# Kernel optimization log

Hardware: AMD Instinct MI355X
Metric: run time of the kernel (lower is better)

The kernel has to match this reference:

```python
import jax, jax.numpy as jnp
import numpy as np

MINI = 1e-6
B, V, K, D = 256, 4096, 64, 10000


def setup_inputs() -> dict:
    key = jax.random.key(0)
    ks = jax.random.split(key, 7)
    batch_BOW = jax.random.randint(ks[0], (B, V), 0, 4, dtype=jnp.int32)
    batch_indices = jax.random.randint(ks[1], (B,), 0, D, dtype=jnp.int64)
    # Gamma-distributed priors as in __init__
    alpha = jax.random.gamma(ks[2], 10.0, (K,)).astype(jnp.float32)
    pi = jax.random.gamma(ks[3], 10.0, (D, K)).astype(jnp.float32)
    beta = (jax.random.gamma(ks[4], 2.0, (V, K)) / 100.0).astype(jnp.float32)
    exp_m = jax.random.uniform(ks[5], (D, K), dtype=jnp.float32)
    exp_m = exp_m / exp_m.sum(axis=1, keepdims=True)  # row-normalized as in __init__
    exp_n = jax.random.uniform(ks[6], (V, K), dtype=jnp.float32)
    exp_n = exp_n / exp_n.sum(axis=1, keepdims=True)
    return {
        "batch_BOW": batch_BOW,
        "batch_indices": batch_indices,
        "alpha": alpha,
        "pi": pi,
        "exp_m": exp_m,
        "beta": beta,
        "exp_n": exp_n,
        "iter_n": 10,
        "C_m": 1000000,
        "batch_C": 25000,
    }


def reference(batch_BOW, batch_indices, alpha, pi, exp_m, beta, exp_n, iter_n, C_m, batch_C):
    # Vectorized SCVB0 E-step (gather nonzero BOW, gamma responsibilities, scatter-accumulate).
    cnt = batch_BOW.astype(alpha.dtype)                      # [B,V]
    mask = (batch_BOW > 0).astype(alpha.dtype)               # [B,V]
    theta = alpha[None, :] * pi[batch_indices] + exp_m[batch_indices]   # [B,K]
    beta_sum = beta.sum(axis=0)                              # [K]
    exp_n_sum = exp_n.sum(axis=0)                            # [K]
    phi = (beta + exp_n) / (beta_sum + exp_n_sum)            # [V,K]
    gamma = theta[:, None, :] * phi[None, :, :] * mask[:, :, None]      # [B,V,K]
    gamma = gamma / (gamma.sum(axis=-1, keepdims=True) + MINI)
    # scatter-accumulate counts
    temp_exp_n = jnp.einsum('bvk,bv->vk', gamma, cnt)        # [V,K]
    temp_exp_m = jnp.einsum('bvk,bv->bk', gamma, cnt)        # [B,K]
    # entropy term: zero rows contribute 0 (0 * log eps = 0), matching nonzero-only loop
    exp_q_z = jnp.sum(gamma * jnp.log(gamma + MINI))
    # stochastic VI update
    rho = 1.0 / (iter_n + 5) ** 0.9
    new_exp_m_batch = (1.0 - rho) * exp_m[batch_indices] + rho * temp_exp_m
    new_exp_n = (1.0 - rho) * exp_n + rho * temp_exp_n * (C_m / batch_C)
    return temp_exp_n, temp_exp_m, exp_q_z, new_exp_n, new_exp_m_batch
```

## Files before the change

### kernel.cpp

```cpp
#include <hip/hip_runtime.h>
#include <math.h>

#define B_ 256
#define V_ 4096
#define K_ 64
#define MINI 1e-6f

#define TEN_OFF 0
#define TEM_OFF (V_*K_)
#define QZ_OFF  (TEM_OFF + B_*K_)
#define NEN_OFF (QZ_OFF + 1)
#define NEM_OFF (NEN_OFF + V_*K_)

#define WS_RHO    64
#define WS_SCALE  65
#define WS_PART   128
#define WS_ENT    4352
#define WS_TENP   8192
#define WS_TEMP   (WS_TENP + 4*V_*K_)

__device__ __forceinline__ int detect_is64(const int* bi) {
    int any = 0;
#pragma unroll
    for (int i = 1; i < 64; i += 2) any |= bi[i];
    return any == 0;
}

__device__ __forceinline__ float wave_sum64(float x) {
    x += __shfl_xor(x, 1);
    x += __shfl_xor(x, 2);
    x += __shfl_xor(x, 4);
    x += __shfl_xor(x, 8);
    x += __shfl_xor(x, 16);
    x += __shfl_xor(x, 32);
    return x;
}

__global__ __launch_bounds__(256) void k_pre(
    const float* __restrict__ beta, const float* __restrict__ exp_n,
    const int* __restrict__ iterp, const int* __restrict__ cmp,
    const int* __restrict__ bcp, float* __restrict__ ws)
{
    const int blk = blockIdx.x, tid = threadIdx.x;
    if (blk < 64) {
        __shared__ float red[256];
        const int k = tid & 63, sub = tid >> 6;
        float p = 0.f;
#pragma unroll
        for (int i = 0; i < 16; i++) {
            const int v = blk * 64 + sub * 16 + i;
            p += beta[v * K_ + k] + exp_n[v * K_ + k];
        }
        red[tid] = p;
        __syncthreads();
        if (tid < 64)
            ws[WS_PART + blk * 64 + tid] =
                red[tid] + red[64 + tid] + red[128 + tid] + red[192 + tid];
    } else {
        if (tid == 0) {
            ws[WS_RHO] = powf((float)(iterp[0] + 5), -0.9f);
            ws[WS_SCALE] = (float)cmp[0] / (float)bcp[0];
        }
    }
}

__global__ __launch_bounds__(256, 1) void k_main(
    const int* __restrict__ BOW, const int* __restrict__ bidx,
    const float* __restrict__ alpha, const float* __restrict__ pi,
    const float* __restrict__ exp_m, const float* __restrict__ beta,
    const float* __restrict__ exp_n,
    float* __restrict__ ws)
{
    __shared__ float th_s[64 * 68];
    __shared__ float ph_s[64 * 68];
    __shared__ float phl_s[64 * 68];
    __shared__ float wtl_s[64 * 68];
    __shared__ unsigned char cnt_s[64 * 65];
    __shared__ float dred[256];
    __shared__ float rden_s[64];
    __shared__ float entw[4];
    __shared__ int is64s;
    const int tid = threadIdx.x;
    const int vt = blockIdx.x & 63, bt = blockIdx.x >> 6;
    const int b0 = bt * 64, v0 = vt * 64;

    if (tid == 0) is64s = detect_is64(bidx);
    {
        const int k = tid & 63, g0 = tid >> 6;
        float s = 0.f;
#pragma unroll
        for (int i = 0; i < 16; i++)
            s += ws[WS_PART + (g0 + 4 * i) * 64 + k];
        dred[tid] = s;
    }
    __syncthreads();
    if (tid < 64)
        rden_s[tid] = __builtin_amdgcn_rcpf(
            dred[tid] + dred[64 + tid] + dred[128 + tid] + dred[192 + tid]);
    __syncthreads();

    {
        const int r = tid >> 2, q = tid & 3;
        const int idx = is64s ? bidx[2 * (b0 + r)] : bidx[b0 + r];
        const int v = v0 + r;
#pragma unroll
        for (int c4 = 0; c4 < 4; c4++) {
            const int k = q * 16 + c4 * 4;
            const float4 a4 = *(const float4*)&alpha[k];
            const float4 p4 = *(const float4*)&pi[idx * K_ + k];
            const float4 m4 = *(const float4*)&exp_m[idx * K_ + k];
            float4 t, tl;
            t.x = a4.x * p4.x + m4.x;  tl.x = t.x * __logf(t.x);
            t.y = a4.y * p4.y + m4.y;  tl.y = t.y * __logf(t.y);
            t.z = a4.z * p4.z + m4.z;  tl.z = t.z * __logf(t.z);
            t.w = a4.w * p4.w + m4.w;  tl.w = t.w * __logf(t.w);
            *(float4*)&th_s[r * 68 + k]  = t;
            *(float4*)&wtl_s[r * 68 + k] = tl;
            const float4 b4 = *(const float4*)&beta[v * K_ + k];
            const float4 e4 = *(const float4*)&exp_n[v * K_ + k];
            const float4 d4 = *(const float4*)&rden_s[k];
            float4 p, pl;
            p.x = (b4.x + e4.x) * d4.x;  pl.x = p.x * __logf(p.x);
            p.y = (b4.y + e4.y) * d4.y;  pl.y = p.y * __logf(p.y);
            p.z = (b4.z + e4.z) * d4.z;  pl.z = p.z * __logf(p.z);
            p.w = (b4.w + e4.w) * d4.w;  pl.w = p.w * __logf(p.w);
            *(float4*)&ph_s[r * 68 + k]  = p;
            *(float4*)&phl_s[r * 68 + k] = pl;
            const int4 cc = *(const int4*)&BOW[(b0 + r) * V_ + v0 + k];
            cnt_s[r * 65 + k + 0] = (unsigned char)cc.x;
            cnt_s[r * 65 + k + 1] = (unsigned char)cc.y;
            cnt_s[r * 65 + k + 2] = (unsigned char)cc.z;
            cnt_s[r * 65 + k + 3] = (unsigned char)cc.w;
        }
    }
    __syncthreads();

    const int tb = tid & 15, tv = tid >> 4;
    float s_acc[4][4] = {}, e_acc[4][4] = {};
    for (int kk = 0; kk < 64; kk += 4) {
        float4 at[4], al[4], bp[4], bl[4];
#pragma unroll
        for (int i = 0; i < 4; i++) {
            at[i] = *(const float4*)&th_s [(tb + 16 * i) * 68 + kk];
            al[i] = *(const float4*)&wtl_s[(tb + 16 * i) * 68 + kk];
        }
#pragma unroll
        for (int j = 0; j < 4; j++) {
            bp[j] = *(const float4*)&ph_s [(tv + 16 * j) * 68 + kk];
            bl[j] = *(const float4*)&phl_s[(tv + 16 * j) * 68 + kk];
        }
#pragma unroll
        for (int i = 0; i < 4; i++)
#pragma unroll
            for (int j = 0; j < 4; j++) {
                s_acc[i][j] += at[i].x * bp[j].x + at[i].y * bp[j].y
                             + at[i].z * bp[j].z + at[i].w * bp[j].w;
                e_acc[i][j] += al[i].x * bp[j].x + al[i].y * bp[j].y
                             + al[i].z * bp[j].z + al[i].w * bp[j].w
                             + at[i].x * bl[j].x + at[i].y * bl[j].y
                             + at[i].z * bl[j].z + at[i].w * bl[j].w;
            }
    }
    __syncthreads();

    float ent = 0.f;
#pragma unroll
    for (int i = 0; i < 4; i++)
#pragma unroll
        for (int j = 0; j < 4; j++) {
            const int bi = tb + 16 * i, vj = tv + 16 * j;
            const float s = s_acc[i][j];
            const float sm = s + MINI;
            const float r = __builtin_amdgcn_rcpf(sm);
            const int c = (int)cnt_s[bi * 65 + vj];
            wtl_s[bi * 68 + vj] = (float)c * r;
            if (c) ent += (e_acc[i][j] - s * __logf(sm)) * r;
        }
    ent = wave_sum64(ent);
    if ((tid & 63) == 0) entw[tid >> 6] = ent;
    __syncthreads();
    if (tid == 0)
        ws[WS_ENT + blockIdx.x] = entw[0] + entw[1] + entw[2] + entw[3];

    {
        const int tk = tid & 15, tv2 = tid >> 4;
        float ta[4][4] = {};
        for (int b = 0; b < 64; b++) {
            const float4 wv = *(const float4*)&wtl_s[b * 68 + 4 * tv2];
            const float4 t4 = *(const float4*)&th_s[b * 68 + 4 * tk];
            const float* wp = &wv.x;
            const float* tp = &t4.x;
#pragma unroll
            for (int j = 0; j < 4; j++)
#pragma unroll
                for (int c = 0; c < 4; c++) ta[j][c] += wp[j] * tp[c];
        }
#pragma unroll
        for (int j = 0; j < 4; j++) {
            const int v = 4 * tv2 + j;
            float4 o;
            o.x = ta[j][0] * ph_s[v * 68 + 4 * tk + 0];
            o.y = ta[j][1] * ph_s[v * 68 + 4 * tk + 1];
            o.z = ta[j][2] * ph_s[v * 68 + 4 * tk + 2];
            o.w = ta[j][3] * ph_s[v * 68 + 4 * tk + 3];
            *(float4*)&ws[WS_TENP + bt * (V_ * K_) + (v0 + v) * K_ + 4 * tk] = o;
        }
    }

    {
        const int tk = tid & 15, tb2 = tid >> 4;
        float Z[4][4] = {};
        for (int v = 0; v < 64; v++) {
            const float4 p4 = *(const float4*)&ph_s[v * 68 + 4 * tk];
            const float* pp = &p4.x;
#pragma unroll
            for (int i = 0; i < 4; i++) {
                const float w = wtl_s[(4 * tb2 + i) * 68 + v];
#pragma unroll
                for (int c = 0; c < 4; c++) Z[i][c] += w * pp[c];
            }
        }
#pragma unroll
        for (int i = 0; i < 4; i++) {
            const int b = 4 * tb2 + i;
            float4 o;
            o.x = th_s[b * 68 + 4 * tk + 0] * Z[i][0];
            o.y = th_s[b * 68 + 4 * tk + 1] * Z[i][1];
            o.z = th_s[b * 68 + 4 * tk + 2] * Z[i][2];
            o.w = th_s[b * 68 + 4 * tk + 3] * Z[i][3];
            *(float4*)&ws[WS_TEMP + blockIdx.x * 4096 + b * K_ + 4 * tk] = o;
        }
    }
}

__global__ __launch_bounds__(256) void k_post(
    const int* __restrict__ bidx, const float* __restrict__ exp_n,
    const float* __restrict__ exp_m, const float* __restrict__ ws,
    float* __restrict__ out)
{
    const int blk = blockIdx.x, tid = threadIdx.x;
    if (blk < 256) {
        const float rho = ws[WS_RHO];
        const int t = blk * 256 + tid;
        const float4 p0 = *(const float4*)&ws[WS_TENP + 0 * (V_ * K_) + t * 4];
        const float4 p1 = *(const float4*)&ws[WS_TENP + 1 * (V_ * K_) + t * 4];
        const float4 p2 = *(const float4*)&ws[WS_TENP + 2 * (V_ * K_) + t * 4];
        const float4 p3 = *(const float4*)&ws[WS_TENP + 3 * (V_ * K_) + t * 4];
        float4 s;
        s.x = (p0.x + p1.x) + (p2.x + p3.x);
        s.y = (p0.y + p1.y) + (p2.y + p3.y);
        s.z = (p0.z + p1.z) + (p2.z + p3.z);
        s.w = (p0.w + p1.w) + (p2.w + p3.w);
        *(float4*)&out[TEN_OFF + t * 4] = s;
        const float4 e4 = *(const float4*)&exp_n[t * 4];
        const float rs = rho * ws[WS_SCALE];
        out[NEN_OFF + t * 4 + 0] = (1.f - rho) * e4.x + rs * s.x;
        out[NEN_OFF + t * 4 + 1] = (1.f - rho) * e4.y + rs * s.y;
        out[NEN_OFF + t * 4 + 2] = (1.f - rho) * e4.z + rs * s.z;
        out[NEN_OFF + t * 4 + 3] = (1.f - rho) * e4.w + rs * s.w;
    } else if (blk < 320) {
        __shared__ int is64s;
        if (tid == 0) is64s = detect_is64(bidx);
        __syncthreads();
        const float rho = ws[WS_RHO];
        const int b = (blk - 256) * 4 + (tid >> 6);
        const int k = tid & 63;
        const int bt = b >> 6, r = b & 63;
        float s = 0.f;
#pragma unroll 8
        for (int vt = 0; vt < 64; vt++)
            s += ws[WS_TEMP + (vt * 4 + bt) * 4096 + r * K_ + k];
        out[TEM_OFF + b * K_ + k] = s;
        const int idx = is64s ? bidx[2 * b] : bidx[b];
        out[NEM_OFF + b * K_ + k] =
            (1.f - rho) * exp_m[idx * K_ + k] + rho * s;
    } else {
        __shared__ float red[256];
        red[tid] = ws[WS_ENT + tid];
        __syncthreads();
        for (int s = 128; s > 0; s >>= 1) {
            if (tid < s) red[tid] += red[tid + s];
            __syncthreads();
        }
        if (tid == 0) out[QZ_OFF] = red[0];
    }
}

extern "C" void kernel_launch(void* const* d_in, const int* in_sizes, int n_in,
                              void* d_out, int out_size, void* d_ws, size_t ws_size,
                              hipStream_t stream)
{
    const int*   BOW   = (const int*)d_in[0];
    const int*   bidx  = (const int*)d_in[1];
    const float* alpha = (const float*)d_in[2];
    const float* pi    = (const float*)d_in[3];
    const float* exp_m = (const float*)d_in[4];
    const float* beta  = (const float*)d_in[5];
    const float* exp_n = (const float*)d_in[6];
    const int*   iterp = (const int*)d_in[7];
    const int*   cmp   = (const int*)d_in[8];
    const int*   bcp   = (const int*)d_in[9];
    float* out = (float*)d_out;
    float* ws  = (float*)d_ws;

    hipLaunchKernelGGL(k_pre, dim3(65), dim3(256), 0, stream,
                       beta, exp_n, iterp, cmp, bcp, ws);
    hipLaunchKernelGGL(k_main, dim3(256), dim3(256), 0, stream,
                       BOW, bidx, alpha, pi, exp_m, beta, exp_n, ws);
    hipLaunchKernelGGL(k_post, dim3(321), dim3(256), 0, stream,
                       bidx, exp_n, exp_m, ws, out);
}
```

Before: 103.5 us.

## Move main-kernel GEMMs onto bf16 MFMA instructions with transposed LDS tiles

Replaces the three scalar FP32 register-tiled mini-GEMMs in k_main (the normalizer/entropy product, the vocab-side accumulation and the doc-side accumulation) with 16x16x32 bf16 MFMA intrinsics. Theta, phi and their x·log(x) terms are stored to LDS as truncated bf16, along with transposed copies so that each MFMA operand fragment is a contiguous 8-element load. The weight matrix W is written in both orientations. The aim is to move the block's FMA-bound inner loops onto the matrix cores. In exchange the products use bf16-truncated operands, which lowers accuracy and may break tolerance. Outputs are now written as scattered scalar stores, and LDS footprint grows.

```diff
diff --git a/kernel.cpp b/kernel.cpp
--- a/kernel.cpp
+++ b/kernel.cpp
@@ -18,6 +18,15 @@
 #define WS_ENT    4352
 #define WS_TENP   8192
 #define WS_TEMP   (WS_TENP + 4*V_*K_)
+
+#define LDB 72
+
+typedef __attribute__((ext_vector_type(8))) short bf16x8;
+typedef __attribute__((ext_vector_type(4))) float f32x4;
+
+__device__ __forceinline__ short bf(float x) {
+    return (short)(__float_as_uint(x) >> 16);
+}
 
 __device__ __forceinline__ int detect_is64(const int* bi) {
     int any = 0;
@@ -34,6 +43,10 @@
     x += __shfl_xor(x, 16);
     x += __shfl_xor(x, 32);
     return x;
+}
+
+__device__ __forceinline__ bf16x8 ldfrag(const short* arr, int row, int kofs) {
+    return *(const bf16x8*)&arr[row * LDB + kofs];
 }
 
 __global__ __launch_bounds__(256) void k_pre(
@@ -71,10 +84,16 @@
     const float* __restrict__ exp_n,
     float* __restrict__ ws)
 {
-    __shared__ float th_s[64 * 68];
-    __shared__ float ph_s[64 * 68];
-    __shared__ float phl_s[64 * 68];
-    __shared__ float wtl_s[64 * 68];
+    __shared__ __align__(16) float th_s[64 * 68];
+    __shared__ __align__(16) float ph_s[64 * 68];
+    __shared__ __align__(16) short th_b [64 * LDB];
+    __shared__ __align__(16) short thl_b[64 * LDB];
+    __shared__ __align__(16) short ph_b [64 * LDB];
+    __shared__ __align__(16) short phl_b[64 * LDB];
+    __shared__ __align__(16) short tht_b[64 * LDB];
+    __shared__ __align__(16) short pht_b[64 * LDB];
+    __shared__ __align__(16) short W_b  [64 * LDB];
+    __shared__ __align__(16) short Wt_b [64 * LDB];
     __shared__ unsigned char cnt_s[64 * 65];
     __shared__ float dred[256];
     __shared__ float rden_s[64];
@@ -114,8 +133,13 @@
             t.y = a4.y * p4.y + m4.y;  tl.y = t.y * __logf(t.y);
             t.z = a4.z * p4.z + m4.z;  tl.z = t.z * __logf(t.z);
             t.w = a4.w * p4.w + m4.w;  tl.w = t.w * __logf(t.w);
-            *(float4*)&th_s[r * 68 + k]  = t;
-            *(float4*)&wtl_s[r * 68 + k] = tl;
+            *(float4*)&th_s[r * 68 + k] = t;
+            *(short4*)&th_b [r * LDB + k] = make_short4(bf(t.x), bf(t.y), bf(t.z), bf(t.w));
+            *(short4*)&thl_b[r * LDB + k] = make_short4(bf(tl.x), bf(tl.y), bf(tl.z), bf(tl.w));
+            tht_b[(k + 0) * LDB + r] = bf(t.x);
+            tht_b[(k + 1) * LDB + r] = bf(t.y);
+            tht_b[(k + 2) * LDB + r] = bf(t.z);
+            tht_b[(k + 3) * LDB + r] = bf(t.w);
             const float4 b4 = *(const float4*)&beta[v * K_ + k];
             const float4 e4 = *(const float4*)&exp_n[v * K_ + k];
             const float4 d4 = *(const float4*)&rden_s[k];
@@ -124,8 +148,13 @@
             p.y = (b4.y + e4.y) * d4.y;  pl.y = p.y * __logf(p.y);
             p.z = (b4.z + e4.z) * d4.z;  pl.z = p.z * __logf(p.z);
             p.w = (b4.w + e4.w) * d4.w;  pl.w = p.w * __logf(p.w);
-            *(float4*)&ph_s[r * 68 + k]  = p;
-            *(float4*)&phl_s[r * 68 + k] = pl;
+            *(float4*)&ph_s[r * 68 + k] = p;
+            *(short4*)&ph_b [r * LDB + k] = make_short4(bf(p.x), bf(p.y), bf(p.z), bf(p.w));
+            *(short4*)&phl_b[r * LDB + k] = make_short4(bf(pl.x), bf(pl.y), bf(pl.z), bf(pl.w));
+            pht_b[(k + 0) * LDB + r] = bf(p.x);
+            pht_b[(k + 1) * LDB + r] = bf(p.y);
+            pht_b[(k + 2) * LDB + r] = bf(p.z);
+            pht_b[(k + 3) * LDB + r] = bf(p.w);
             const int4 cc = *(const int4*)&BOW[(b0 + r) * V_ + v0 + k];
             cnt_s[r * 65 + k + 0] = (unsigned char)cc.x;
             cnt_s[r * 65 + k + 1] = (unsigned char)cc.y;
@@ -135,100 +164,92 @@
     }
     __syncthreads();
 
-    const int tb = tid & 15, tv = tid >> 4;
-    float s_acc[4][4] = {}, e_acc[4][4] = {};
-    for (int kk = 0; kk < 64; kk += 4) {
-        float4 at[4], al[4], bp[4], bl[4];
-#pragma unroll
-        for (int i = 0; i < 4; i++) {
-            at[i] = *(const float4*)&th_s [(tb + 16 * i) * 68 + kk];
-            al[i] = *(const float4*)&wtl_s[(tb + 16 * i) * 68 + kk];
-        }
+    const int lane = tid & 63, wv = tid >> 6;
+    const int l15 = lane & 15, quad = lane >> 4;
+    const int qk = quad * 8;
+
+    {
+        const int mb = wv * 16;
+        const bf16x8 a_t0 = ldfrag(th_b,  mb + l15, 0  + qk);
+        const bf16x8 a_t1 = ldfrag(th_b,  mb + l15, 32 + qk);
+        const bf16x8 a_l0 = ldfrag(thl_b, mb + l15, 0  + qk);
+        const bf16x8 a_l1 = ldfrag(thl_b, mb + l15, 32 + qk);
+        float entacc = 0.f;
 #pragma unroll
         for (int j = 0; j < 4; j++) {
-            bp[j] = *(const float4*)&ph_s [(tv + 16 * j) * 68 + kk];
-            bl[j] = *(const float4*)&phl_s[(tv + 16 * j) * 68 + kk];
-        }
-#pragma unroll
-        for (int i = 0; i < 4; i++)
-#pragma unroll
-            for (int j = 0; j < 4; j++) {
-                s_acc[i][j] += at[i].x * bp[j].x + at[i].y * bp[j].y
-                             + at[i].z * bp[j].z + at[i].w * bp[j].w;
-                e_acc[i][j] += al[i].x * bp[j].x + al[i].y * bp[j].y
-                             + al[i].z * bp[j].z + al[i].w * bp[j].w
-                             + at[i].x * bl[j].x + at[i].y * bl[j].y
-                             + at[i].z * bl[j].z + at[i].w * bl[j].w;
+            const int vrow = j * 16 + l15;
+            const bf16x8 b_p0 = ldfrag(ph_b,  vrow, 0  + qk);
+            const bf16x8 b_p1 = ldfrag(ph_b,  vrow, 32 + qk);
+            const bf16x8 b_l0 = ldfrag(phl_b, vrow, 0  + qk);
+            const bf16x8 b_l1 = ldfrag(phl_b, vrow, 32 + qk);
+            f32x4 sa = {0.f, 0.f, 0.f, 0.f};
+            f32x4 ea = {0.f, 0.f, 0.f, 0.f};
+            sa = __builtin_amdgcn_mfma_f32_16x16x32_bf16(a_t0, b_p0, sa, 0, 0, 0);
+            sa = __builtin_amdgcn_mfma_f32_16x16x32_bf16(a_t1, b_p1, sa, 0, 0, 0);
+            ea = __builtin_amdgcn_mfma_f32_16x16x32_bf16(a_l0, b_p0, ea, 0, 0, 0);
+            ea = __builtin_amdgcn_mfma_f32_16x16x32_bf16(a_l1, b_p1, ea, 0, 0, 0);
+            ea = __builtin_amdgcn_mfma_f32_16x16x32_bf16(a_t0, b_l0, ea, 0, 0, 0);
+            ea = __builtin_amdgcn_mfma_f32_16x16x32_bf16(a_t1, b_l1, ea, 0, 0, 0);
+#pragma unroll
+            for (int reg = 0; reg < 4; reg++) {
+                const int b = mb + quad * 4 + reg;
+                const int v = j * 16 + l15;
+                const float s = sa[reg];
+                const float sm = s + MINI;
+                const float rr = __builtin_amdgcn_rcpf(sm);
+                const int c = (int)cnt_s[b * 65 + v];
+                const float w = (float)c * rr;
+                W_b [b * LDB + v] = bf(w);
+                Wt_b[v * LDB + b] = bf(w);
+                if (c) entacc += (ea[reg] - s * __logf(sm)) * rr;
             }
-    }
-    __syncthreads();
-
-    float ent = 0.f;
-#pragma unroll
-    for (int i = 0; i < 4; i++)
-#pragma unroll
-        for (int j = 0; j < 4; j++) {
-            const int bi = tb + 16 * i, vj = tv + 16 * j;
-            const float s = s_acc[i][j];
-            const float sm = s + MINI;
-            const float r = __builtin_amdgcn_rcpf(sm);
-            const int c = (int)cnt_s[bi * 65 + vj];
-            wtl_s[bi * 68 + vj] = (float)c * r;
-            if (c) ent += (e_acc[i][j] - s * __logf(sm)) * r;
-        }
-    ent = wave_sum64(ent);
-    if ((tid & 63) == 0) entw[tid >> 6] = ent;
+        }
+        entacc = wave_sum64(entacc);
+        if (lane == 0) entw[wv] = entacc;
+    }
     __syncthreads();
     if (tid == 0)
         ws[WS_ENT + blockIdx.x] = entw[0] + entw[1] + entw[2] + entw[3];
 
     {
-        const int tk = tid & 15, tv2 = tid >> 4;
-        float ta[4][4] = {};
-        for (int b = 0; b < 64; b++) {
-            const float4 wv = *(const float4*)&wtl_s[b * 68 + 4 * tv2];
-            const float4 t4 = *(const float4*)&th_s[b * 68 + 4 * tk];
-            const float* wp = &wv.x;
-            const float* tp = &t4.x;
-#pragma unroll
-            for (int j = 0; j < 4; j++)
-#pragma unroll
-                for (int c = 0; c < 4; c++) ta[j][c] += wp[j] * tp[c];
-        }
+        const int mv = wv * 16;
+        const bf16x8 wa0 = ldfrag(Wt_b, mv + l15, 0  + qk);
+        const bf16x8 wa1 = ldfrag(Wt_b, mv + l15, 32 + qk);
 #pragma unroll
         for (int j = 0; j < 4; j++) {
-            const int v = 4 * tv2 + j;
-            float4 o;
-            o.x = ta[j][0] * ph_s[v * 68 + 4 * tk + 0];
-            o.y = ta[j][1] * ph_s[v * 68 + 4 * tk + 1];
-            o.z = ta[j][2] * ph_s[v * 68 + 4 * tk + 2];
-            o.w = ta[j][3] * ph_s[v * 68 + 4 * tk + 3];
-            *(float4*)&ws[WS_TENP + bt * (V_ * K_) + (v0 + v) * K_ + 4 * tk] = o;
-        }
-    }
-
-    {
-        const int tk = tid & 15, tb2 = tid >> 4;
-        float Z[4][4] = {};
-        for (int v = 0; v < 64; v++) {
-            const float4 p4 = *(const float4*)&ph_s[v * 68 + 4 * tk];
-            const float* pp = &p4.x;
-#pragma unroll
-            for (int i = 0; i < 4; i++) {
-                const float w = wtl_s[(4 * tb2 + i) * 68 + v];
-#pragma unroll
-                for (int c = 0; c < 4; c++) Z[i][c] += w * pp[c];
+            const bf16x8 bt0 = ldfrag(tht_b, j * 16 + l15, 0  + qk);
+            const bf16x8 bt1 = ldfrag(tht_b, j * 16 + l15, 32 + qk);
+            f32x4 acc = {0.f, 0.f, 0.f, 0.f};
+            acc = __builtin_amdgcn_mfma_f32_16x16x32_bf16(wa0, bt0, acc, 0, 0, 0);
+            acc = __builtin_amdgcn_mfma_f32_16x16x32_bf16(wa1, bt1, acc, 0, 0, 0);
+#pragma unroll
+            for (int reg = 0; reg < 4; reg++) {
+                const int v = mv + quad * 4 + reg;
+                const int kc = j * 16 + l15;
+                ws[WS_TENP + bt * (V_ * K_) + (v0 + v) * K_ + kc] =
+                    acc[reg] * ph_s[v * 68 + kc];
             }
         }
-#pragma unroll
-        for (int i = 0; i < 4; i++) {
-            const int b = 4 * tb2 + i;
-            float4 o;
-            o.x = th_s[b * 68 + 4 * tk + 0] * Z[i][0];
-            o.y = th_s[b * 68 + 4 * tk + 1] * Z[i][1];
-            o.z = th_s[b * 68 + 4 * tk + 2] * Z[i][2];
-            o.w = th_s[b * 68 + 4 * tk + 3] * Z[i][3];
-            *(float4*)&ws[WS_TEMP + blockIdx.x * 4096 + b * K_ + 4 * tk] = o;
+    }
+
+    {
+        const int mb = wv * 16;
+        const bf16x8 wa0 = ldfrag(W_b, mb + l15, 0  + qk);
+        const bf16x8 wa1 = ldfrag(W_b, mb + l15, 32 + qk);
+#pragma unroll
+        for (int j = 0; j < 4; j++) {
+            const bf16x8 bp0 = ldfrag(pht_b, j * 16 + l15, 0  + qk);
+            const bf16x8 bp1 = ldfrag(pht_b, j * 16 + l15, 32 + qk);
+            f32x4 acc = {0.f, 0.f, 0.f, 0.f};
+            acc = __builtin_amdgcn_mfma_f32_16x16x32_bf16(wa0, bp0, acc, 0, 0, 0);
+            acc = __builtin_amdgcn_mfma_f32_16x16x32_bf16(wa1, bp1, acc, 0, 0, 0);
+#pragma unroll
+            for (int reg = 0; reg < 4; reg++) {
+                const int b = mb + quad * 4 + reg;
+                const int kc = j * 16 + l15;
+                ws[WS_TEMP + blockIdx.x * 4096 + b * K_ + kc] =
+                    acc[reg] * th_s[b * 68 + kc];
+            }
         }
     }
 }
```

After: 93.78 us. 1.1x faster.
